# Performance work log

Hardware: AMD Instinct MI355X
Metric: run time of the kernel (lower is better)

Reference implementation:

```python
import jax, jax.numpy as jnp
import numpy as np


def setup_inputs() -> dict:
    key = jax.random.key(0)
    kx, kd = jax.random.split(key)
    B, T, C = 32, 512, 512
    x = jax.random.normal(kx, (B, T, C), dtype=jnp.float32)
    dur = jax.random.randint(kd, (B, T), 0, 12, dtype=jnp.int32)
    return {"x": x, "dur": dur}


def reference(x, dur):
    # x: [B, T, C]; dur: [B, T] integer per-token durations.
    # Equivalent of the torch CPU double-loop: output frame t of row b
    # takes source index j where cumsum(dur)[b, j-1] <= t < cumsum(dur)[b, j];
    # frames past the total duration repeat the last source index (T-1).
    dur = jnp.maximum(dur, 0)
    cum = jnp.cumsum(dur, axis=1)                       # [B, T], nondecreasing
    T_out = int(jnp.max(cum))                            # data-dependent output length (eager)
    frames = jnp.arange(T_out, dtype=cum.dtype)          # [T_out]
    # searchsorted(cum[b], t, 'right') == first j with cum[b, j] > t
    idx = jax.vmap(lambda c: jnp.searchsorted(c, frames, side="right"))(cum)  # [B, T_out]
    idx = jnp.minimum(idx, x.shape[1] - 1)               # overflow -> last token, matches torch loop
    return jnp.take_along_axis(x, idx[:, :, None], axis=1)  # [B, T_out, C]
```

## Files before the change

kernel.cpp:

```cpp
#include <hip/hip_runtime.h>
#include <hip/hip_bf16.h>


#define LR_T 512

__global__ void lr_cumsum_kernel(const int* __restrict__ dur,
                                 int* __restrict__ cum, int T) {
    __shared__ int s[LR_T];
    const int b = blockIdx.x;
    const int tid = threadIdx.x;
    int v = dur[(size_t)b * T + tid];
    v = v > 0 ? v : 0;
    s[tid] = v;
    __syncthreads();
    for (int off = 1; off < LR_T; off <<= 1) {
        int add = (tid >= off) ? s[tid - off] : 0;
        __syncthreads();
        s[tid] += add;
        __syncthreads();
    }
    cum[(size_t)b * T + tid] = s[tid];
}

__global__ void __launch_bounds__(128)
lr_scatter_kernel(const float4* __restrict__ x4,
                  const int* __restrict__ cum,
                  float4* __restrict__ out4,
                  int T, int T_out) {
    const int j = blockIdx.x;
    const int b = blockIdx.y;
    const int tid = threadIdx.x;

    const int* crow = cum + (size_t)b * T;
    int start = (j > 0) ? crow[j - 1] : 0;
    int end   = (j == T - 1) ? T_out : crow[j];
    if (start >= end) return;

    const float4 val = x4[((size_t)b * T + j) * 128 + tid];

    float4* dst = out4 + ((size_t)b * T_out + start) * 128 + tid;
    for (int t = start; t < end; ++t) {
        *dst = val;
        dst += 128;
    }
}

extern "C" void kernel_launch(void* const* d_in, const int* in_sizes, int n_in,
                              void* d_out, int out_size, void* d_ws, size_t ws_size,
                              hipStream_t stream) {
    const float* x   = (const float*)d_in[0];
    const int*   dur = (const int*)d_in[1];
    float*       out = (float*)d_out;

    const int B  = 32;
    const int BT = in_sizes[1];
    const int T  = BT / B;
    const int C  = in_sizes[0] / BT;
    const int T_out = out_size / (B * C);

    int* cum = (int*)d_ws;

    lr_cumsum_kernel<<<B, T, 0, stream>>>(dur, cum, T);

    dim3 grid(T, B);
    lr_scatter_kernel<<<grid, 128, 0, stream>>>(
        (const float4*)x, cum, (float4*)out, T, T_out);
}
```

Baseline: 246.1 us.

## Split tail padding across extra blocks and use nontemporal wide stores

Adds NTAIL extra blocks per batch row that share the overflow tail (frames past a row's total duration, which repeat the last token). Previously a single block wrote that whole tail serially. Each block now runs 256 threads, so two output frames are written per iteration. Loads and stores use nontemporal builtins to avoid polluting the cache on the streaming write. Launch overhead grows with more blocks, and most tail blocks exit early when the tail is short.

```diff
diff --git a/kernel.cpp b/kernel.cpp
--- a/kernel.cpp
+++ b/kernel.cpp
@@ -2,7 +2,10 @@
 #include <hip/hip_bf16.h>
 
 
-#define LR_T 512
+#define LR_T   512
+#define NTAIL  64
+
+typedef float vfloat4 __attribute__((ext_vector_type(4)));
 
 __global__ void lr_cumsum_kernel(const int* __restrict__ dur,
                                  int* __restrict__ cum, int T) {
@@ -22,26 +25,44 @@
     cum[(size_t)b * T + tid] = s[tid];
 }
 
-__global__ void __launch_bounds__(128)
-lr_scatter_kernel(const float4* __restrict__ x4,
+__global__ void __launch_bounds__(256)
+lr_scatter_kernel(const vfloat4* __restrict__ x4,
                   const int* __restrict__ cum,
-                  float4* __restrict__ out4,
+                  vfloat4* __restrict__ out4,
                   int T, int T_out) {
-    const int j = blockIdx.x;
-    const int b = blockIdx.y;
-    const int tid = threadIdx.x;
+    const int jj   = blockIdx.x;
+    const int b    = blockIdx.y;
+    const int tid  = threadIdx.x;
+    const int lane = tid & 127;
+    const int half = tid >> 7;
 
     const int* crow = cum + (size_t)b * T;
-    int start = (j > 0) ? crow[j - 1] : 0;
-    int end   = (j == T - 1) ? T_out : crow[j];
+    int j, start, end;
+    if (jj < T) {
+        j     = jj;
+        start = (jj > 0) ? crow[jj - 1] : 0;
+        end   = crow[jj];
+    } else {
+        j = T - 1;
+        const int tstart = crow[T - 1];
+        const int tlen   = T_out - tstart;
+        if (tlen <= 0) return;
+        const int chunk = (tlen + NTAIL - 1) / NTAIL;
+        const int k     = jj - T;
+        start = tstart + k * chunk;
+        end   = start + chunk;
+        if (end > T_out) end = T_out;
+    }
     if (start >= end) return;
 
-    const float4 val = x4[((size_t)b * T + j) * 128 + tid];
+    const vfloat4 val =
+        __builtin_nontemporal_load(&x4[((size_t)b * T + j) * 128 + lane]);
 
-    float4* dst = out4 + ((size_t)b * T_out + start) * 128 + tid;
-    for (int t = start; t < end; ++t) {
-        *dst = val;
-        dst += 128;
+    vfloat4* const base = out4 + (size_t)b * T_out * 128 + lane;
+    vfloat4* dst = base + ((size_t)start + half) * 128;
+    for (int t = start + half; t < end; t += 2) {
+        __builtin_nontemporal_store(val, dst);
+        dst += 256;
     }
 }
 
@@ -62,7 +83,7 @@
 
     lr_cumsum_kernel<<<B, T, 0, stream>>>(dur, cum, T);
 
-    dim3 grid(T, B);
-    lr_scatter_kernel<<<grid, 128, 0, stream>>>(
-        (const float4*)x, cum, (float4*)out, T, T_out);
+    dim3 grid(T + NTAIL, B);
+    lr_scatter_kernel<<<grid, 256, 0, stream>>>(
+        (const vfloat4*)x, cum, (vfloat4*)out, T, T_out);
 }
```

Result: faster. 231.8 us (-5.8%).
